# Kernel tuning notes

Measured on AMD Instinct MI355X. Metric: run time of the kernel, lower is better.

Reference implementation:

```python
import jax, jax.numpy as jnp
import numpy as np

H = 64            # hidden_dim
N_NODES = 100000
N_EDGES = 2000000
IN_DIM = 2 * H + 2  # src_emb || dst_emb || src_fiedler || dst_fiedler


def setup_inputs() -> dict:
    key = jax.random.key(0)
    ks = jax.random.split(key, 10)
    node_embeddings = jax.random.normal(ks[0], (N_NODES, H), dtype=jnp.float32)
    edge_index = jax.random.randint(ks[1], (2, N_EDGES), 0, N_NODES, dtype=jnp.int64)
    fiedler_vector = jax.random.normal(ks[2], (N_NODES,), dtype=jnp.float32)
    # MLP scorer params: Linear(130,64)+ReLU, Linear(64,64)+ReLU, Linear(64,1)
    def lin(k, fan_in, fan_out):
        bound = 1.0 / np.sqrt(fan_in)
        kw, kb = jax.random.split(k)
        W = jax.random.uniform(kw, (fan_in, fan_out), jnp.float32, -bound, bound)
        b = jax.random.uniform(kb, (fan_out,), jnp.float32, -bound, bound)
        return W, b
    W1, b1 = lin(ks[3], IN_DIM, H)
    W2, b2 = lin(ks[4], H, H)
    W3, b3 = lin(ks[5], H, 1)
    return {
        "node_embeddings": node_embeddings,
        "fiedler_vector": fiedler_vector,
        "W1": W1, "b1": b1, "W2": W2, "b2": b2, "W3": W3, "b3": b3,
        "edge_index": edge_index,
        "num_nodes": N_NODES,
    }


def reference(node_embeddings, fiedler_vector, W1, b1, W2, b2, W3, b3, edge_index, num_nodes):
    src, dst = edge_index[0], edge_index[1]
    # Gather + concat edge features: [E, 2H+2]
    feats = jnp.concatenate(
        [
            node_embeddings[src],               # [E, H]
            node_embeddings[dst],               # [E, H]
            fiedler_vector[src][:, None],        # [E, 1]
            fiedler_vector[dst][:, None],        # [E, 1]
        ],
        axis=-1,
    )
    # Edge scorer MLP (Dropout is identity in eval mode)
    h = jax.nn.relu(feats @ W1 + b1)
    h = jax.nn.relu(h @ W2 + b2)
    edge_scores = (h @ W3 + b3)[:, 0]  # [E]
    return edge_scores
```

## Files before the change

### kernel.cpp

```cpp
#include <hip/hip_runtime.h>


#define HD 64

typedef __attribute__((ext_vector_type(8))) _Float16 half8;
typedef __attribute__((ext_vector_type(4))) _Float16 half4;
typedef __attribute__((ext_vector_type(8))) short  short8;
typedef __attribute__((ext_vector_type(8))) float  float8;
typedef __attribute__((ext_vector_type(4))) float  f32x4;

__device__ __forceinline__ half8 relu_h8(half8 x) {
    short8 b = __builtin_bit_cast(short8, x);
    short8 m = b >> 15;
    b = b & ~m;
    return __builtin_bit_cast(half8, b);
}

__global__ __launch_bounds__(256) void precompute_uv(
    const float* __restrict__ emb, const float* __restrict__ fied,
    const float* __restrict__ W1, const float* __restrict__ b1,
    _Float16* __restrict__ u, _Float16* __restrict__ v,
    int n_nodes, int ntiles)
{
    const int lane = threadIdx.x & 63;
    const int q = lane >> 4;
    const int c = lane & 15;
    const int wid = blockIdx.x * (blockDim.x >> 6) + (threadIdx.x >> 6);
    const int nw  = gridDim.x * (blockDim.x >> 6);

    half8 Au[4][2], Av[4][2];
    #pragma unroll
    for (int t = 0; t < 4; ++t)
        #pragma unroll
        for (int ks = 0; ks < 2; ++ks)
            #pragma unroll
            for (int j = 0; j < 8; ++j) {
                int k = ks * 32 + q * 8 + j;
                Au[t][ks][j] = (_Float16)W1[k * HD + t * 16 + c];
                Av[t][ks][j] = (_Float16)W1[(64 + k) * HD + t * 16 + c];
            }
    f32x4 b1q[4], wsq[4], wdq[4];
    #pragma unroll
    for (int t = 0; t < 4; ++t) {
        b1q[t] = *(const f32x4*)(b1 + t * 16 + q * 4);
        wsq[t] = *(const f32x4*)(W1 + 128 * HD + t * 16 + q * 4);
        wdq[t] = *(const f32x4*)(W1 + 129 * HD + t * 16 + q * 4);
    }

    for (int tile = wid; tile < ntiles; tile += nw) {
        const int n0 = tile * 16;
        const int n  = n0 + c;
        int na = n; if (na >= n_nodes) na = n_nodes - 1;
        const float* rp = emb + (size_t)na * HD + q * 8;
        float8 a0 = *(const float8*)rp;
        float8 a1 = *(const float8*)(rp + 32);
        half8 B0 = __builtin_convertvector(a0, half8);
        half8 B1 = __builtin_convertvector(a1, half8);

        f32x4 aU[4] = {}, aV[4] = {};
        #pragma unroll
        for (int t = 0; t < 4; ++t) {
            aU[t] = __builtin_amdgcn_mfma_f32_16x16x32_f16(Au[t][0], B0, aU[t], 0, 0, 0);
            aU[t] = __builtin_amdgcn_mfma_f32_16x16x32_f16(Au[t][1], B1, aU[t], 0, 0, 0);
            aV[t] = __builtin_amdgcn_mfma_f32_16x16x32_f16(Av[t][0], B0, aV[t], 0, 0, 0);
            aV[t] = __builtin_amdgcn_mfma_f32_16x16x32_f16(Av[t][1], B1, aV[t], 0, 0, 0);
        }

        const float fv = fied[na];
        const bool ok = (n < n_nodes);
        #pragma unroll
        for (int t = 0; t < 4; ++t) {
            half4 hu, hv;
            #pragma unroll
            for (int r = 0; r < 4; ++r) {
                hu[r] = (_Float16)(aU[t][r] + b1q[t][r] + fv * wsq[t][r]);
                hv[r] = (_Float16)(aV[t][r] + fv * wdq[t][r]);
            }
            if (ok) {
                *(half4*)(u + (size_t)n * HD + t * 16 + q * 4) = hu;
                *(half4*)(v + (size_t)n * HD + t * 16 + q * 4) = hv;
            }
        }
    }
}

__global__ __launch_bounds__(256) void edge_mlp(
    const _Float16* __restrict__ u, const _Float16* __restrict__ v,
    const int* __restrict__ src, const int* __restrict__ dst,
    const float* __restrict__ W2, const float* __restrict__ b2,
    const float* __restrict__ W3, const float* __restrict__ b3,
    float* __restrict__ out, int E, int ntiles)
{
    const int lane = threadIdx.x & 63;
    const int q = lane >> 4;
    const int c = lane & 15;
    const int wid = blockIdx.x * (blockDim.x >> 6) + (threadIdx.x >> 6);
    const int nw  = gridDim.x * (blockDim.x >> 6);

    half8 Af[4][2];
    #pragma unroll
    for (int t = 0; t < 4; ++t)
        #pragma unroll
        for (int ks = 0; ks < 2; ++ks)
            #pragma unroll
            for (int j = 0; j < 8; ++j) {
                int k = ks * 32 + q * 8 + j;
                Af[t][ks][j] = (_Float16)W2[k * HD + t * 16 + c];
            }
    f32x4 b2q[4], w3q[4];
    #pragma unroll
    for (int t = 0; t < 4; ++t) {
        b2q[t] = *(const f32x4*)(b2 + t * 16 + q * 4);
        w3q[t] = *(const f32x4*)(W3 + t * 16 + q * 4);
    }
    const float b3v = b3[0];

    const int stride = nw * 2;
    const int base0  = wid * 2;

    auto eid = [&](int tile) {
        int t = tile; if (t >= ntiles) t = ntiles - 1;
        int e = t * 16 + c; if (e >= E) e = E - 1;
        return e;
    };
    auto issue = [&](int s, int d, half8& Ua, half8& Ub, half8& Va, half8& Vb) {
        const half8* up = (const half8*)(u + (unsigned)s * HD + q * 8);
        const half8* vp = (const half8*)(v + (unsigned)d * HD + q * 8);
        Ua = up[0]; Ub = up[4]; Va = vp[0]; Vb = vp[4];
    };
    auto compute_store = [&](int tile, half8 Ua, half8 Ub, half8 Va, half8 Vb) {
        half8 B0 = relu_h8(Ua + Va);
        half8 B1 = relu_h8(Ub + Vb);
        f32x4 acc[4] = {};
        #pragma unroll
        for (int t = 0; t < 4; ++t) {
            acc[t] = __builtin_amdgcn_mfma_f32_16x16x32_f16(Af[t][0], B0, acc[t], 0, 0, 0);
            acc[t] = __builtin_amdgcn_mfma_f32_16x16x32_f16(Af[t][1], B1, acc[t], 0, 0, 0);
        }
        float p = 0.f;
        #pragma unroll
        for (int t = 0; t < 4; ++t)
            #pragma unroll
            for (int r = 0; r < 4; ++r)
                p = fmaf(fmaxf(acc[t][r] + b2q[t][r], 0.f), w3q[t][r], p);
        p += __shfl_xor(p, 16, 64);
        p += __shfl_xor(p, 32, 64);
        if (q == 0) {
            int e = tile * 16 + c;
            if (e < E) out[e] = p + b3v;
        }
    };

    if (base0 >= ntiles) return;

    int e0 = eid(base0), e1 = eid(base0 + 1);
    int s0 = src[e0], d0 = dst[e0];
    int s1 = src[e1], d1 = dst[e1];
    half8 U0a, U0b, V0a, V0b, U1a, U1b, V1a, V1b;
    issue(s0, d0, U0a, U0b, V0a, V0b);
    issue(s1, d1, U1a, U1b, V1a, V1b);
    int e2 = eid(base0 + stride), e3 = eid(base0 + stride + 1);
    int sc0 = src[e2], dc0 = dst[e2];
    int sc1 = src[e3], dc1 = dst[e3];

    for (int base = base0; base < ntiles; base += stride) {
        const int f0 = eid(base + 2 * stride), f1 = eid(base + 2 * stride + 1);
        const int sn0 = src[f0], dn0 = dst[f0];
        const int sn1 = src[f1], dn1 = dst[f1];

        compute_store(base, U0a, U0b, V0a, V0b);
        issue(sc0, dc0, U0a, U0b, V0a, V0b);

        compute_store(base + 1, U1a, U1b, V1a, V1b);
        issue(sc1, dc1, U1a, U1b, V1a, V1b);

        sc0 = sn0; dc0 = dn0; sc1 = sn1; dc1 = dn1;
    }
}

extern "C" void kernel_launch(void* const* d_in, const int* in_sizes, int n_in,
                              void* d_out, int out_size, void* d_ws, size_t ws_size,
                              hipStream_t stream) {
    const float* emb  = (const float*)d_in[0];
    const float* fied = (const float*)d_in[1];
    const float* W1   = (const float*)d_in[2];
    const float* b1   = (const float*)d_in[3];
    const float* W2   = (const float*)d_in[4];
    const float* b2   = (const float*)d_in[5];
    const float* W3   = (const float*)d_in[6];
    const float* b3   = (const float*)d_in[7];
    const int*   eidx = (const int*)d_in[8];

    const int n_nodes = in_sizes[1];
    const int E       = in_sizes[8] / 2;
    const int* srcp = eidx;
    const int* dstp = eidx + E;

    _Float16* u = (_Float16*)d_ws;
    _Float16* v = u + (size_t)n_nodes * HD;

    const int ntilesN = (n_nodes + 15) / 16;
    precompute_uv<<<1024, 256, 0, stream>>>(emb, fied, W1, b1, u, v,
                                            n_nodes, ntilesN);

    const int ntilesE = (E + 15) / 16;
    edge_mlp<<<2048, 256, 0, stream>>>(u, v, srcp, dstp, W2, b2, W3, b3,
                                       (float*)d_out, E, ntilesE);
}
```

Baseline: 175.9 us.

## Bucket edges by src/dst node range before edge MLP for gather locality

Adds a counting-sort pass (histogram, per-bucket scan, base offsets, scatter) that groups edges into 64 buckets by source and destination node range. Each edge becomes a packed 64-bit record holding src, dst and its original edge id. A new edge kernel assigns blocks to source-range groups so the u/v gathers hit a smaller working set that fits better in cache. The bias b2 is also folded into the MFMA accumulator init. The cost is four extra kernel launches plus writing and reading 16 MB of records per call, and the output is now stored scattered instead of coalesced.

```diff
diff --git a/kernel.cpp b/kernel.cpp
--- a/kernel.cpp
+++ b/kernel.cpp
@@ -131,7 +131,9 @@
     auto compute_store = [&](int tile, half8 Ua, half8 Ub, half8 Va, half8 Vb) {
         half8 B0 = relu_h8(Ua + Va);
         half8 B1 = relu_h8(Ub + Vb);
-        f32x4 acc[4] = {};
+        f32x4 acc[4];
+        #pragma unroll
+        for (int t = 0; t < 4; ++t) acc[t] = b2q[t];
         #pragma unroll
         for (int t = 0; t < 4; ++t) {
             acc[t] = __builtin_amdgcn_mfma_f32_16x16x32_f16(Af[t][0], B0, acc[t], 0, 0, 0);
@@ -142,7 +144,7 @@
         for (int t = 0; t < 4; ++t)
             #pragma unroll
             for (int r = 0; r < 4; ++r)
-                p = fmaf(fmaxf(acc[t][r] + b2q[t][r], 0.f), w3q[t][r], p);
+                p = fmaf(fmaxf(acc[t][r], 0.f), w3q[t][r], p);
         p += __shfl_xor(p, 16, 64);
         p += __shfl_xor(p, 32, 64);
         if (q == 0) {
@@ -175,6 +177,202 @@
         issue(sc1, dc1, U1a, U1b, V1a, V1b);
 
         sc0 = sn0; dc0 = dn0; sc1 = sn1; dc1 = dn1;
+    }
+}
+
+#define NCH 2048
+
+__global__ __launch_bounds__(256) void hist_k(
+    const int* __restrict__ src, const int* __restrict__ dst,
+    unsigned* __restrict__ counts, int E, int CH, unsigned mul8)
+{
+    __shared__ unsigned h[64];
+    const int b = blockIdx.x;
+    for (int i = threadIdx.x; i < 64; i += 256) h[i] = 0u;
+    __syncthreads();
+    const int lo = b * CH;
+    int hi = lo + CH; if (hi > E) hi = E;
+    for (int i = lo + threadIdx.x; i < hi; i += 256) {
+        unsigned s = (unsigned)src[i], d = (unsigned)dst[i];
+        unsigned bk = __umulhi(s, mul8) * 8u + __umulhi(d, mul8);
+        atomicAdd(&h[bk], 1u);
+    }
+    __syncthreads();
+    for (int i = threadIdx.x; i < 64; i += 256) counts[(size_t)b * 64 + i] = h[i];
+}
+
+__global__ __launch_bounds__(256) void scanb_k(
+    unsigned* __restrict__ counts, unsigned* __restrict__ totals)
+{
+    __shared__ unsigned part[256];
+    const int bk = blockIdx.x;
+    const int t  = threadIdx.x;
+    unsigned vpre[8];
+    unsigned sum = 0u;
+    const int c0 = t * 8;
+    #pragma unroll
+    for (int j = 0; j < 8; ++j) {
+        unsigned x = counts[(size_t)(c0 + j) * 64 + bk];
+        vpre[j] = sum; sum += x;
+    }
+    part[t] = sum;
+    __syncthreads();
+    for (int d = 1; d < 256; d <<= 1) {
+        unsigned x = (t >= d) ? part[t - d] : 0u;
+        __syncthreads();
+        part[t] += x;
+        __syncthreads();
+    }
+    const unsigned incl = part[t];
+    const unsigned excl = incl - sum;
+    #pragma unroll
+    for (int j = 0; j < 8; ++j)
+        counts[(size_t)(c0 + j) * 64 + bk] = vpre[j] + excl;
+    if (t == 255) totals[bk] = incl;
+}
+
+__global__ __launch_bounds__(64) void base_k(
+    const unsigned* __restrict__ totals, unsigned* __restrict__ base)
+{
+    const int t = threadIdx.x;
+    const unsigned own = totals[t];
+    unsigned x = own;
+    #pragma unroll
+    for (int d = 1; d < 64; d <<= 1) {
+        unsigned y = __shfl_up(x, d, 64);
+        if (t >= d) x += y;
+    }
+    base[t] = x - own;
+    if (t == 63) base[64] = x;
+}
+
+__global__ __launch_bounds__(256) void scat_k(
+    const int* __restrict__ src, const int* __restrict__ dst,
+    const unsigned* __restrict__ counts, const unsigned* __restrict__ base,
+    unsigned long long* __restrict__ recs, int E, int CH, unsigned mul8)
+{
+    __shared__ unsigned cur[64];
+    const int b = blockIdx.x;
+    for (int i = threadIdx.x; i < 64; i += 256)
+        cur[i] = base[i] + counts[(size_t)b * 64 + i];
+    __syncthreads();
+    const int lo = b * CH;
+    int hi = lo + CH; if (hi > E) hi = E;
+    for (int i = lo + threadIdx.x; i < hi; i += 256) {
+        unsigned s = (unsigned)src[i], d = (unsigned)dst[i];
+        unsigned bk = __umulhi(s, mul8) * 8u + __umulhi(d, mul8);
+        unsigned slot = atomicAdd(&cur[bk], 1u);
+        recs[slot] = (unsigned long long)s
+                   | ((unsigned long long)d << 17)
+                   | ((unsigned long long)(unsigned)i << 34);
+    }
+}
+
+__global__ __launch_bounds__(256) void edge_mlp_b(
+    const _Float16* __restrict__ u, const _Float16* __restrict__ v,
+    const unsigned long long* __restrict__ recs,
+    const unsigned* __restrict__ boff,
+    const float* __restrict__ W2, const float* __restrict__ b2,
+    const float* __restrict__ W3, const float* __restrict__ b3,
+    float* __restrict__ out)
+{
+    const int lane = threadIdx.x & 63;
+    const int q = lane >> 4;
+    const int c = lane & 15;
+
+    const int x   = blockIdx.x & 7;
+    const int lb  = blockIdx.x >> 3;
+    const int nlb = gridDim.x >> 3;
+
+    const unsigned rs = boff[x * 8];
+    const unsigned re = boff[x * 8 + 8];
+    if (re <= rs) return;
+    const int ntiles = (int)((re - rs + 15u) >> 4);
+
+    half8 Af[4][2];
+    #pragma unroll
+    for (int t = 0; t < 4; ++t)
+        #pragma unroll
+        for (int ks = 0; ks < 2; ++ks)
+            #pragma unroll
+            for (int j = 0; j < 8; ++j) {
+                int k = ks * 32 + q * 8 + j;
+                Af[t][ks][j] = (_Float16)W2[k * HD + t * 16 + c];
+            }
+    f32x4 b2q[4], w3q[4];
+    #pragma unroll
+    for (int t = 0; t < 4; ++t) {
+        b2q[t] = *(const f32x4*)(b2 + t * 16 + q * 4);
+        w3q[t] = *(const f32x4*)(W3 + t * 16 + q * 4);
+    }
+    const float b3v = b3[0];
+
+    const int wid = lb * ((int)blockDim.x >> 6) + (threadIdx.x >> 6);
+    const int nw  = nlb * ((int)blockDim.x >> 6);
+    const int stride = nw * 2;
+    const int base0  = wid * 2;
+    if (base0 >= ntiles) return;
+
+    auto ridx = [&](int tile) -> unsigned {
+        int t = tile; if (t >= ntiles) t = ntiles - 1;
+        unsigned r = rs + (unsigned)t * 16u + (unsigned)c;
+        if (r >= re) r = re - 1u;
+        return r;
+    };
+    auto issue = [&](unsigned s, unsigned d, half8& Ua, half8& Ub, half8& Va, half8& Vb) {
+        const half8* up = (const half8*)(u + (unsigned)s * HD + q * 8);
+        const half8* vp = (const half8*)(v + (unsigned)d * HD + q * 8);
+        Ua = up[0]; Ub = up[4]; Va = vp[0]; Vb = vp[4];
+    };
+    auto compute_store = [&](int tile, unsigned eid,
+                             half8 Ua, half8 Ub, half8 Va, half8 Vb) {
+        half8 B0 = relu_h8(Ua + Va);
+        half8 B1 = relu_h8(Ub + Vb);
+        f32x4 acc[4];
+        #pragma unroll
+        for (int t = 0; t < 4; ++t) acc[t] = b2q[t];
+        #pragma unroll
+        for (int t = 0; t < 4; ++t) {
+            acc[t] = __builtin_amdgcn_mfma_f32_16x16x32_f16(Af[t][0], B0, acc[t], 0, 0, 0);
+            acc[t] = __builtin_amdgcn_mfma_f32_16x16x32_f16(Af[t][1], B1, acc[t], 0, 0, 0);
+        }
+        float p = 0.f;
+        #pragma unroll
+        for (int t = 0; t < 4; ++t)
+            #pragma unroll
+            for (int r = 0; r < 4; ++r)
+                p = fmaf(fmaxf(acc[t][r], 0.f), w3q[t][r], p);
+        p += __shfl_xor(p, 16, 64);
+        p += __shfl_xor(p, 32, 64);
+        if (q == 0 && (rs + (unsigned)tile * 16u + (unsigned)c) < re)
+            out[eid] = p + b3v;
+    };
+
+    unsigned long long r0 = recs[ridx(base0)];
+    unsigned long long r1 = recs[ridx(base0 + 1)];
+    unsigned e0 = (unsigned)(r0 >> 34);
+    unsigned e1 = (unsigned)(r1 >> 34);
+    half8 U0a, U0b, V0a, V0b, U1a, U1b, V1a, V1b;
+    issue((unsigned)r0 & 0x1FFFFu, (unsigned)(r0 >> 17) & 0x1FFFFu, U0a, U0b, V0a, V0b);
+    issue((unsigned)r1 & 0x1FFFFu, (unsigned)(r1 >> 17) & 0x1FFFFu, U1a, U1b, V1a, V1b);
+    unsigned long long rc0 = recs[ridx(base0 + stride)];
+    unsigned long long rc1 = recs[ridx(base0 + stride + 1)];
+
+    for (int bse = base0; bse < ntiles; bse += stride) {
+        const unsigned long long rn0 = recs[ridx(bse + 2 * stride)];
+        const unsigned long long rn1 = recs[ridx(bse + 2 * stride + 1)];
+
+        compute_store(bse, e0, U0a, U0b, V0a, V0b);
+        e0 = (unsigned)(rc0 >> 34);
+        issue((unsigned)rc0 & 0x1FFFFu, (unsigned)(rc0 >> 17) & 0x1FFFFu,
+              U0a, U0b, V0a, V0b);
+
+        compute_store(bse + 1, e1, U1a, U1b, V1a, V1b);
+        e1 = (unsigned)(rc1 >> 34);
+        issue((unsigned)rc1 & 0x1FFFFu, (unsigned)(rc1 >> 17) & 0x1FFFFu,
+              U1a, U1b, V1a, V1b);
+
+        rc0 = rn0; rc1 = rn1;
     }
 }
 
@@ -198,12 +396,39 @@
 
     _Float16* u = (_Float16*)d_ws;
     _Float16* v = u + (size_t)n_nodes * HD;
+    const size_t uv_bytes = (size_t)n_nodes * HD * 2 * sizeof(_Float16);
 
     const int ntilesN = (n_nodes + 15) / 16;
     precompute_uv<<<1024, 256, 0, stream>>>(emb, fied, W1, b1, u, v,
                                             n_nodes, ntilesN);
 
-    const int ntilesE = (E + 15) / 16;
-    edge_mlp<<<2048, 256, 0, stream>>>(u, v, srcp, dstp, W2, b2, W3, b3,
-                                       (float*)d_out, E, ntilesE);
-}
+    const size_t recs_off   = uv_bytes;
+    const size_t counts_off = recs_off + (size_t)E * 8;
+    const size_t totals_off = counts_off + (size_t)NCH * 64 * 4;
+    const size_t base_off   = totals_off + 64 * 4;
+    const size_t need       = base_off + 65 * 4;
+
+    const bool can_bucket = (ws_size >= need) &&
+                            (n_nodes <= 131072) && (n_nodes >= 4096) &&
+                            ((long long)E < (1LL << 30));
+
+    if (can_bucket) {
+        unsigned long long* recs = (unsigned long long*)((char*)d_ws + recs_off);
+        unsigned* counts = (unsigned*)((char*)d_ws + counts_off);
+        unsigned* totals = (unsigned*)((char*)d_ws + totals_off);
+        unsigned* basep  = (unsigned*)((char*)d_ws + base_off);
+        const unsigned mul8 = (unsigned)((8ULL << 32) / (unsigned long long)n_nodes);
+        const int CH = (E + NCH - 1) / NCH;
+
+        hist_k <<<NCH, 256, 0, stream>>>(srcp, dstp, counts, E, CH, mul8);
+        scanb_k<<<64,  256, 0, stream>>>(counts, totals);
+        base_k <<<1,    64, 0, stream>>>(totals, basep);
+        scat_k <<<NCH, 256, 0, stream>>>(srcp, dstp, counts, basep, recs, E, CH, mul8);
+        edge_mlp_b<<<2048, 256, 0, stream>>>(u, v, recs, basep,
+                                             W2, b2, W3, b3, (float*)d_out);
+    } else {
+        const int ntilesE = (E + 15) / 16;
+        edge_mlp<<<2048, 256, 0, stream>>>(u, v, srcp, dstp, W2, b2, W3, b3,
+                                           (float*)d_out, E, ntilesE);
+    }
+}
```

Result: slower. 204.7 us (+16.4%).
